# Performance work log

Measured on AMD Instinct MI355X. Metric: run time of the kernel, lower is better.

The kernel has to match this reference:

```python
import jax, jax.numpy as jnp
import numpy as np

HEAD_NUM = 16
NEG_BIG = -2.0**32 + 1.0


def _pos_encoding(T, D):
    pos = np.arange(T)[:, None].astype(np.float64)
    i = np.arange(D)[None, :].astype(np.float64)
    angle = pos / np.power(10000.0, 2.0 * i / D)
    pe = np.empty((T, D), dtype=np.float64)
    pe[:, 0::2] = np.sin(angle[:, 0::2])
    pe[:, 1::2] = np.cos(angle[:, 1::2])
    return jnp.asarray(pe * (D ** 0.5), dtype=jnp.float32)  # scale=True


def setup_inputs() -> dict:
    key = jax.random.key(0)
    ks = jax.random.split(key, 9)
    B, T, D = 32, 512, 1024
    return {
        "queries": jax.random.normal(ks[0], (B, T, D), jnp.float32),
        "keys": jax.random.normal(ks[1], (B, T, D), jnp.float32),
        "query_masks": jax.random.randint(ks[2], (B, 1), 1, T + 1, jnp.int32),
        "key_masks": jax.random.randint(ks[3], (B, 1), 1, T + 1, jnp.int32),
        "W_Query": jax.random.normal(ks[4], (D, D), jnp.float32) * 0.02,
        "W_key": jax.random.normal(ks[5], (D, D), jnp.float32) * 0.02,
        "W_Value": jax.random.normal(ks[6], (D, D), jnp.float32) * 0.02,
        "fw1": jax.random.normal(ks[7], (D, 4 * D), jnp.float32) * 0.02,
        "fw2": jax.random.normal(ks[8], (4 * D, D), jnp.float32) * 0.02,
    }


def reference(queries, keys, query_masks, key_masks, W_Query, W_key, W_Value, fw1, fw2):
    B, T, D = queries.shape
    h = HEAD_NUM
    d = D // h
    pe = _pos_encoding(T, D)  # [T, D]

    # faithful to source: queries get PE; keys = PE(queries_with_PE) (keys input unused)
    q_pe = queries + pe[None]
    k_pe = q_pe + pe[None]

    qs = jnp.einsum('btd,de->bte', q_pe, W_Query)
    ks_ = jnp.einsum('btd,de->bte', k_pe, W_key)
    vs = jnp.einsum('btd,de->bte', ks_, W_Value)  # faithful: values from projected keys

    def split_heads(x):  # [B,T,h*d] -> [h,B,T,d] (matches tf.split/concat on axis 0)
        return x.reshape(B, T, h, d).transpose(2, 0, 1, 3)

    q4, k4, v4 = split_heads(qs), split_heads(ks_), split_heads(vs)

    scores = jnp.einsum('hbqd,hbkd->hbqk', q4, k4) / (d ** 0.5)

    pos = jnp.arange(T)
    km = (pos[None, :] < key_masks).astype(jnp.float32)    # [B,T]
    qm = (pos[None, :] < query_masks).astype(jnp.float32)  # [B,T]

    scores = jnp.where(km[None, :, None, :] == 1.0, scores, NEG_BIG)
    scores = scores - jnp.max(scores, axis=-1, keepdims=True)
    attn = jax.nn.softmax(scores, axis=-1)
    attn = attn * qm[None, :, :, None]

    out = jnp.einsum('hbqk,hbkd->hbqd', attn, v4)
    result = out.transpose(1, 2, 0, 3).reshape(B, T, D)  # merge heads (head-major)

    result = result + q_pe  # use_res
    # feed forward (use_layer_norm=False, no dropout at inference)
    hmid = jax.nn.relu(jnp.einsum('btd,df->btf', result, fw1))
    result = result + jnp.einsum('btf,fd->btd', hmid, fw2)

    # output_type == 'mean'
    return jnp.mean(result, axis=1, keepdims=True)  # [B,1,D]
```

## Files before the change

kernel.cpp:

```cpp
#include <hip/hip_runtime.h>

constexpr int B_  = 32;
constexpr int T_  = 512;
constexpr int D_  = 1024;
constexpr int NH_ = 16;
constexpr int DH_ = 64;
constexpr int F_  = 4096;
constexpr int BT_ = B_ * T_;

typedef __attribute__((ext_vector_type(8))) short bf16x8;
typedef __attribute__((ext_vector_type(4))) float f32x4;

#define DEVI __device__ __forceinline__

DEVI unsigned short f2bf(float f) {
  union { float f; unsigned u; } uf; uf.f = f;
  unsigned r = uf.u + 0x7fffu + ((uf.u >> 16) & 1u);
  return (unsigned short)(r >> 16);
}
DEVI float b2f(unsigned short h) {
  union { unsigned u; float f; } uf; uf.u = ((unsigned)h) << 16;
  return uf.f;
}
DEVI void gload16(const void* g, void* l) {
  __builtin_amdgcn_global_load_lds(
      (const __attribute__((address_space(1))) void*)(uintptr_t)g,
      (__attribute__((address_space(3))) void*)(unsigned)(uintptr_t)l, 16, 0, 0);
}

__global__ void pe_kernel(float* __restrict__ pe) {
  int idx = blockIdx.x * 256 + threadIdx.x;
  int t = idx >> 10, j = idx & 1023;
  float inv = exp2f(-(2.0f * (float)j / 1024.0f) * 13.2877123795494f);
  float ang = (float)t * inv;
  float v = (j & 1) ? cosf(ang) : sinf(ang);
  pe[idx] = v * 32.0f;
}

__global__ void pack_kernel(const float* __restrict__ q, const float* __restrict__ pe,
                            unsigned short* __restrict__ q_pe, unsigned short* __restrict__ k_pe) {
  long i = ((long)blockIdx.x * 256 + threadIdx.x) * 4;
  const float4 qv = *(const float4*)(q + i);
  const float4 pv = *(const float4*)(pe + (i & (long)(T_ * D_ - 1)));
  ushort4 a, b;
  a.x = f2bf(qv.x + pv.x); a.y = f2bf(qv.y + pv.y);
  a.z = f2bf(qv.z + pv.z); a.w = f2bf(qv.w + pv.w);
  b.x = f2bf(qv.x + 2.f * pv.x); b.y = f2bf(qv.y + 2.f * pv.y);
  b.z = f2bf(qv.z + 2.f * pv.z); b.w = f2bf(qv.w + 2.f * pv.w);
  *(ushort4*)(q_pe + i) = a;
  *(ushort4*)(k_pe + i) = b;
}

__global__ void transpose_w(const float* __restrict__ W, unsigned short* __restrict__ Wt,
                            int K, int N) {
  __shared__ float tile[32][33];
  int tx = threadIdx.x & 31, ty = threadIdx.x >> 5;
  int bx = blockIdx.x, by = blockIdx.y;
  for (int i = 0; i < 4; i++) {
    int r = by * 32 + ty + i * 8;
    tile[ty + i * 8][tx] = W[(long)r * N + bx * 32 + tx];
  }
  __syncthreads();
  for (int i = 0; i < 4; i++) {
    int r = bx * 32 + ty + i * 8;
    Wt[(long)r * K + by * 32 + tx] = f2bf(tile[tx][ty + i * 8]);
  }
}

__global__ void cast_bf16(const float* __restrict__ W, unsigned short* __restrict__ Wb) {
  long i = ((long)blockIdx.x * 256 + threadIdx.x) * 4;
  const float4 v = *(const float4*)(W + i);
  ushort4 o;
  o.x = f2bf(v.x); o.y = f2bf(v.y); o.z = f2bf(v.z); o.w = f2bf(v.w);
  *(ushort4*)(Wb + i) = o;
}

template <int EPI>
__global__ __launch_bounds__(256) void gemm_bt(
    const unsigned short* __restrict__ A0, const unsigned short* __restrict__ Bt0,
    unsigned short* __restrict__ C0, float* __restrict__ hacc, int M, int N, int K) {
  __shared__ unsigned short As[128 * 32];
  __shared__ unsigned short Bs[128 * 32];
  const unsigned short* A  = A0;
  const unsigned short* Bt = Bt0;
  unsigned short* C        = C0;

  const int tid = threadIdx.x;
  const int lane = tid & 63, w = tid >> 6;
  const int wr = w >> 1, wc = w & 1;
  const int l15 = lane & 15, lhi = lane >> 4;
  const int brow = blockIdx.y * 128, bcol = blockIdx.x * 128;

  f32x4 acc[4][4] = {};
  const int o = tid * 16;
  const int srow = o >> 6;
  const int skel = (o & 63) >> 1;

  for (int kk = 0; kk < K; kk += 32) {
    gload16(A + (long)(brow + srow) * K + kk + skel,        (char*)As + o);
    gload16(A + (long)(brow + srow + 64) * K + kk + skel,   (char*)As + o + 4096);
    gload16(Bt + (long)(bcol + srow) * K + kk + skel,       (char*)Bs + o);
    gload16(Bt + (long)(bcol + srow + 64) * K + kk + skel,  (char*)Bs + o + 4096);
    __syncthreads();
    bf16x8 af[4], bfr[4];
    for (int m = 0; m < 4; m++)
      af[m] = *(const bf16x8*)((const char*)As + ((wr * 64 + m * 16 + l15) * 64 + lhi * 16));
    for (int n = 0; n < 4; n++)
      bfr[n] = *(const bf16x8*)((const char*)Bs + ((wc * 64 + n * 16 + l15) * 64 + lhi * 16));
    for (int m = 0; m < 4; m++)
      for (int n = 0; n < 4; n++)
        acc[m][n] = __builtin_amdgcn_mfma_f32_16x16x32_bf16(af[m], bfr[n], acc[m][n], 0, 0, 0);
    __syncthreads();
  }

  for (int m = 0; m < 4; m++)
    for (int n = 0; n < 4; n++) {
      int row = brow + wr * 64 + m * 16 + lhi * 4;
      int col = bcol + wc * 64 + n * 16 + l15;
      for (int r = 0; r < 4; r++)
        C[(long)(row + r) * N + col] = f2bf(acc[m][n][r]);
    }
}

template <int EPI>
__global__ __launch_bounds__(512, 2) void gemm8(
    const unsigned short* __restrict__ A0, const unsigned short* __restrict__ Bt0, unsigned short* __restrict__ C0,
    const unsigned short* __restrict__ A1, const unsigned short* __restrict__ Bt1, unsigned short* __restrict__ C1,
    const unsigned short* __restrict__ A2, const unsigned short* __restrict__ Bt2, unsigned short* __restrict__ C2,
    float* __restrict__ hacc, int N,
    const int* __restrict__ L0, const int* __restrict__ L1, const int* __restrict__ L2) {
  constexpr int K = 1024, NK = 16, NI = 8;
  __shared__ char lds[2][2][32768];

  const int z = blockIdx.z;
  const unsigned short* A  = (z == 0) ? A0  : (z == 1 ? A1  : A2);
  const unsigned short* Bt = (z == 0) ? Bt0 : (z == 1 ? Bt1 : Bt2);
  unsigned short* C        = (z == 0) ? C0  : (z == 1 ? C1  : C2);
  const int* L             = (z == 0) ? L0  : (z == 1 ? L1  : L2);

  const long brow = (long)blockIdx.x * 256, bcol = (long)blockIdx.y * 256;
  if (L && (brow & 256) && L[brow >> 9] <= 256) return;

  const int tid = threadIdx.x;
  const int lane = tid & 63, w = tid >> 6;
  const int wm = w >> 2, wn = w & 3;
  const int l15 = lane & 15, lhi = lane >> 4;

  const int drow = (tid * 16) >> 7;
  const int dcol = ((tid * 16) & 127) ^ ((drow & 7) << 4);
  const int sw   = (l15 & 7) << 4;

  f32x4 acc[8][4] = {};
  bf16x8 bfr[4][2], af[2][2];

  auto STAGE = [&](const unsigned short* __restrict__ P, long tb, int kt, int h, int buf, int op) {
    const unsigned short* g = P + (tb + h * 128 + drow) * (long)K + kt * 64 + (dcol >> 1);
    char* l = &lds[buf][op][h * 16384 + tid * 16];
    gload16(g, l);
    gload16(g + 64L * K, l + 8192);
  };
  auto LDA = [&](int buf, int q) {
#pragma unroll
    for (int mi = 0; mi < 2; mi++) {
      int row = wm * 128 + (q * 2 + mi) * 16 + l15;
#pragma unroll
      for (int kk = 0; kk < 2; kk++)
        af[mi][kk] = *(const bf16x8*)(&lds[buf][0][0] + (row << 7) + ((kk * 64 + lhi * 16) ^ sw));
    }
  };
  auto LDB = [&](int buf) {
#pragma unroll
    for (int n = 0; n < 4; n++) {
      int row = wn * 64 + n * 16 + l15;
#pragma unroll
      for (int kk = 0; kk < 2; kk++)
        bfr[n][kk] = *(const bf16x8*)(&lds[buf][1][0] + (row << 7) + ((kk * 64 + lhi * 16) ^ sw));
    }
  };
  auto MFMAQ = [&](int q) {
    __builtin_amdgcn_s_setprio(1);
#pragma unroll
    for (int mi = 0; mi < 2; mi++)
#pragma unroll
      for (int n = 0; n < 4; n++)
#pragma unroll
        for (int kk = 0; kk < 2; kk++)
          acc[q * 2 + mi][n] =
              __builtin_amdgcn_mfma_f32_16x16x32_bf16(af[mi][kk], bfr[n][kk], acc[q * 2 + mi][n], 0, 0, 0);
    __builtin_amdgcn_s_setprio(0);
  };
#define BAR() __builtin_amdgcn_s_barrier()
#define GATE4() asm volatile("s_waitcnt vmcnt(4)" ::: "memory")

  STAGE(A, brow, 0, 0, 0, 0);  STAGE(A, brow, 0, 1, 0, 0);
  STAGE(Bt, bcol, 0, 0, 0, 1); STAGE(Bt, bcol, 0, 1, 0, 1);
  STAGE(Bt, bcol, 1, 0, 1, 1); STAGE(Bt, bcol, 1, 1, 1, 1);
  GATE4();
  BAR();

  for (int i = 0; i < NI; ++i) {
    const int k1 = 2 * i + 1;
    const int ka = (2 * i + 2) & (NK - 1);
    const int kb = (2 * i + 3) & (NK - 1);
    LDA(0, 0); LDB(0); STAGE(A, brow, k1, 0, 1, 0);
    BAR(); MFMAQ(0); BAR();
    LDA(0, 1);         STAGE(A, brow, k1, 1, 1, 0);
    BAR(); MFMAQ(1); BAR();
    LDA(0, 2);         STAGE(Bt, bcol, ka, 0, 0, 1);
    BAR(); MFMAQ(2); BAR();
    LDA(0, 3);         STAGE(Bt, bcol, ka, 1, 0, 1);
    BAR(); MFMAQ(3);
    GATE4();
    BAR();
    LDA(1, 0); LDB(1); STAGE(A, brow, ka, 0, 0, 0);
    BAR(); MFMAQ(0); BAR();
    LDA(1, 1);         STAGE(A, brow, ka, 1, 0, 0);
    BAR(); MFMAQ(1); BAR();
    LDA(1, 2);         STAGE(Bt, bcol, kb, 0, 1, 1);
    BAR(); MFMAQ(2); BAR();
    LDA(1, 3);         STAGE(Bt, bcol, kb, 1, 1, 1);
    BAR(); MFMAQ(3);
    GATE4();
    BAR();
  }
#undef BAR
#undef GATE4

  if (EPI == 0) {
    if (z == 2) {
      char* tl = &lds[0][0][0] + (w << 14);
#pragma unroll
      for (int m = 0; m < 8; m++)
#pragma unroll
        for (int n = 0; n < 4; n++) {
          int cl = n * 16 + l15;
#pragma unroll
          for (int r = 0; r < 4; r++) {
            int tofs = m * 16 + lhi * 4 + r;
            *(unsigned short*)(tl + cl * 256 + ((tofs * 2) ^ ((cl & 7) << 4))) = f2bf(acc[m][n][r]);
          }
        }
      asm volatile("" ::: "memory");
      const int bb = (int)(brow >> 9), t0 = (int)(brow & 511);
#pragma unroll
      for (int rr = 0; rr < 16; rr++) {
        int row = rr * 4 + lhi;
        bf16x8 v = *(const bf16x8*)(tl + row * 256 + ((l15 * 16) ^ ((row & 7) << 4)));
        int gcol = (int)bcol + wn * 64 + row;
        long vtrow = ((long)(bb * NH_ + (gcol >> 6))) * DH_ + (gcol & 63);
        *(bf16x8*)(C + vtrow * T_ + t0 + wm * 128 + l15 * 8) = v;
      }
    } else {
#pragma unroll
      for (int m = 0; m < 8; m++)
#pragma unroll
        for (int n = 0; n < 4; n++) {
          long row = brow + wm * 128 + m * 16 + lhi * 4;
          long col = bcol + wn * 64 + n * 16 + l15;
#pragma unroll
          for (int r = 0; r < 4; r++)
            C[(row + r) * (long)N + col] = f2bf(acc[m][n][r]);
        }
    }
  } else {
    const int batch = (int)(brow >> 9);
#pragma unroll
    for (int n = 0; n < 4; n++) {
      float t = 0.f;
#pragma unroll
      for (int m = 0; m < 8; m++)
#pragma unroll
        for (int r = 0; r < 4; r++) t += fmaxf(acc[m][n][r], 0.f);
      t += __shfl_xor(t, 16);
      t += __shfl_xor(t, 32);
      if (lane < 16)
        atomicAdd(hacc + (long)batch * F_ + bcol + wn * 64 + n * 16 + l15, t);
    }
  }
}

__global__ __launch_bounds__(256, 3) void attn_kernel(
    const unsigned short* __restrict__ qs, const unsigned short* __restrict__ ks,
    const unsigned short* __restrict__ vt, const unsigned short* __restrict__ q_pe,
    const int* __restrict__ qmask, const int* __restrict__ kmask,
    unsigned short* __restrict__ res, float* __restrict__ racc) {
  __shared__ unsigned short Ks[2][64 * 64];
  __shared__ unsigned short Vs[2][64 * 64];
  __shared__ unsigned short Ps[4][32 * 64];

  const int tid = threadIdx.x, lane = tid & 63, w = tid >> 6;
  const int l15 = lane & 15, lhi = lane >> 4;
  const int h = blockIdx.x, b = blockIdx.y, q0 = blockIdx.z * 128;
  const int qlen = qmask[b], kvlen = kmask[b];

  if (q0 >= qlen) {
    int cc = tid & 63;
    float s = 0.f;
    for (int i = 0; i < 32; i++) {
      int r = (tid >> 6) * 32 + i;
      long addr = (long)(b * T_ + q0 + r) * D_ + h * DH_ + cc;
      unsigned short v = q_pe[addr];
      res[addr] = v;
      s += b2f(v);
    }
    atomicAdd(racc + b * D_ + h * DH_ + cc, s);
    return;
  }

  bf16x8 qf[2][2];
  for (int m = 0; m < 2; m++)
    for (int k2 = 0; k2 < 2; k2++) {
      int t = q0 + w * 32 + m * 16 + l15;
      qf[m][k2] = *(const bf16x8*)(qs + (long)(b * T_ + t) * D_ + h * DH_ + k2 * 32 + lhi * 8);
    }

  f32x4 o[2][4] = {};
  float mrun[2][4], lrun[2][4];
  for (int m = 0; m < 2; m++)
    for (int r = 0; r < 4; r++) { mrun[m][r] = -3e38f; lrun[m][r] = 0.f; }

  const float SCL = 0.125f * 1.4426950408889634f;
  const float THR = 8.0f / SCL;
  const int nc = (kvlen + 63) >> 6;

  auto stage = [&](int c, int buf) {
#pragma unroll
    for (int cl = 0; cl < 2; cl++) {
      int ob = cl * 4096 + tid * 16;
      int os = ob ^ (((ob >> 7) & 7) << 4);
      int r0 = os >> 7, cb = os & 127;
      gload16(ks + (long)(b * T_ + c * 64 + r0) * D_ + h * DH_ + (cb >> 1),
              (char*)&Ks[buf][0] + ob);
      gload16(vt + ((long)(b * NH_ + h) * DH_ + r0) * T_ + c * 64 + (cb >> 1),
              (char*)&Vs[buf][0] + ob);
    }
  };

  stage(0, 0);
  int cur = 0;
  for (int c = 0; c < nc; c++) {
    const int nxt = (c + 1 < nc) ? c + 1 : c;
    stage(nxt, cur ^ 1);
    asm volatile("s_waitcnt vmcnt(4)" ::: "memory");
    __builtin_amdgcn_sched_barrier(0);
    __builtin_amdgcn_s_barrier();

    f32x4 s[2][4] = {};
    for (int k2 = 0; k2 < 2; k2++)
      for (int n = 0; n < 4; n++) {
        int key = n * 16 + l15;
        int Ab = key * 128 + (k2 * 32 + lhi * 8) * 2;
        bf16x8 kf = *(const bf16x8*)((const char*)&Ks[cur][0] + (Ab ^ ((key & 7) << 4)));
        s[0][n] = __builtin_amdgcn_mfma_f32_16x16x32_bf16(qf[0][k2], kf, s[0][n], 0, 0, 0);
        s[1][n] = __builtin_amdgcn_mfma_f32_16x16x32_bf16(qf[1][k2], kf, s[1][n], 0, 0, 0);
      }

    if (c == nc - 1) {
      for (int n = 0; n < 4; n++)
        if (c * 64 + n * 16 + l15 >= kvlen)
          for (int m = 0; m < 2; m++) s[m][n] = f32x4{-3e38f, -3e38f, -3e38f, -3e38f};
    }

    for (int m = 0; m < 2; m++) {
      float mx[4];
      for (int r = 0; r < 4; r++) {
        float v = s[m][0][r];
        for (int n = 1; n < 4; n++) v = fmaxf(v, s[m][n][r]);
        mx[r] = v;
      }
      for (int msk = 1; msk < 16; msk <<= 1)
        for (int r = 0; r < 4; r++) mx[r] = fmaxf(mx[r], __shfl_xor(mx[r], msk));
      bool grow = false;
      for (int r = 0; r < 4; r++) grow = grow || (mx[r] > mrun[m][r] + THR);
      if (__any(grow)) {
        float corr[4];
        for (int r = 0; r < 4; r++) {
          float mn = fmaxf(mrun[m][r], mx[r]);
          corr[r] = exp2f((mrun[m][r] - mn) * SCL);
          mrun[m][r] = mn;
        }
        for (int nd = 0; nd < 4; nd++)
          for (int r = 0; r < 4; r++) o[m][nd][r] *= corr[r];
        for (int r = 0; r < 4; r++) lrun[m][r] *= corr[r];
      }
      float ps[4] = {0.f, 0.f, 0.f, 0.f};
      for (int n = 0; n < 4; n++)
        for (int r = 0; r < 4; r++) {
          float pval = exp2f((s[m][n][r] - mrun[m][r]) * SCL);
          s[m][n][r] = pval;
          ps[r] += pval;
        }
      for (int msk = 1; msk < 16; msk <<= 1)
        for (int r = 0; r < 4; r++) ps[r] += __shfl_xor(ps[r], msk);
      for (int r = 0; r < 4; r++) lrun[m][r] += ps[r];
      for (int n = 0; n < 4; n++)
        for (int r = 0; r < 4; r++) {
          int row = m * 16 + lhi * 4 + r;
          int Ab = row * 128 + (n * 16 + l15) * 2;
          *(unsigned short*)((char*)&Ps[w][0] + (Ab ^ ((row & 7) << 4))) = f2bf(s[m][n][r]);
        }
    }
    asm volatile("" ::: "memory");

    for (int k4 = 0; k4 < 2; k4++) {
      bf16x8 pa[2];
      for (int m = 0; m < 2; m++) {
        int row = m * 16 + l15;
        int Ab = row * 128 + k4 * 64 + lhi * 16;
        pa[m] = *(const bf16x8*)((const char*)&Ps[w][0] + (Ab ^ ((row & 7) << 4)));
      }
      for (int nd = 0; nd < 4; nd++) {
        int dv = nd * 16 + l15;
        int Ab = dv * 128 + k4 * 64 + lhi * 16;
        bf16x8 vb = *(const bf16x8*)((const char*)&Vs[cur][0] + (Ab ^ ((dv & 7) << 4)));
        for (int m = 0; m < 2; m++)
          o[m][nd] = __builtin_amdgcn_mfma_f32_16x16x32_bf16(pa[m], vb, o[m][nd], 0, 0, 0);
      }
    }
    __builtin_amdgcn_s_barrier();
    cur ^= 1;
  }

  float cs[4] = {0.f, 0.f, 0.f, 0.f};
  for (int m = 0; m < 2; m++)
    for (int r = 0; r < 4; r++) {
      int t = q0 + w * 32 + m * 16 + lhi * 4 + r;
      float inv = 1.0f / lrun[m][r];
      bool valid = t < qlen;
      for (int nd = 0; nd < 4; nd++) {
        long addr = (long)(b * T_ + t) * D_ + h * DH_ + nd * 16 + l15;
        float v = valid ? o[m][nd][r] * inv : 0.f;
        float val = v + b2f(q_pe[addr]);
        res[addr] = f2bf(val);
        cs[nd] += val;
      }
    }
  for (int nd = 0; nd < 4; nd++) {
    cs[nd] += __shfl_xor(cs[nd], 16);
    cs[nd] += __shfl_xor(cs[nd], 32);
  }
  if (lane < 16)
    for (int nd = 0; nd < 4; nd++)
      atomicAdd(racc + b * D_ + h * DH_ + nd * 16 + l15, cs[nd]);
}

__global__ void final_kernel(const float* __restrict__ hacc, const float* __restrict__ fw2,
                             const float* __restrict__ racc, float* __restrict__ out) {
  int n = blockIdx.x * 64 + (threadIdx.x & 63);
  int bg = threadIdx.x >> 6;
  int f0 = blockIdx.y * 512;
  float acc[8] = {};
  for (int f = f0; f < f0 + 512; f++) {
    float wv = fw2[(long)f * D_ + n];
    for (int i = 0; i < 8; i++) acc[i] += hacc[(long)(bg * 8 + i) * F_ + f] * wv;
  }
  if (blockIdx.y == 0)
    for (int i = 0; i < 8; i++) acc[i] += racc[(long)(bg * 8 + i) * D_ + n];
  for (int i = 0; i < 8; i++)
    atomicAdd(out + (bg * 8 + i) * D_ + n, acc[i] * (1.0f / 512.0f));
}

extern "C" void kernel_launch(void* const* d_in, const int* in_sizes, int n_in,
                              void* d_out, int out_size, void* d_ws, size_t ws_size,
                              hipStream_t stream) {
  const float* queries = (const float*)d_in[0];
  const int*   qmask = (const int*)d_in[2];
  const int*   kmask = (const int*)d_in[3];
  const float* Wq  = (const float*)d_in[4];
  const float* Wk  = (const float*)d_in[5];
  const float* Wv  = (const float*)d_in[6];
  const float* fw1 = (const float*)d_in[7];
  const float* fw2 = (const float*)d_in[8];
  float* out = (float*)d_out;

  char* p = (char*)d_ws;
  auto alloc = [&](size_t bytes) -> char* {
    char* r = p; p += (bytes + 255) & ~(size_t)255; return r;
  };
  float*          pe   = (float*)alloc((size_t)T_ * D_ * 4);
  unsigned short* q_pe = (unsigned short*)alloc((size_t)BT_ * D_ * 2);
  unsigned short* k_pe = (unsigned short*)alloc((size_t)BT_ * D_ * 2);
  unsigned short* qs   = (unsigned short*)alloc((size_t)BT_ * D_ * 2);
  unsigned short* ksb  = (unsigned short*)alloc((size_t)BT_ * D_ * 2);
  unsigned short* vt   = (unsigned short*)alloc((size_t)BT_ * D_ * 2);
  unsigned short* res  = (unsigned short*)alloc((size_t)BT_ * D_ * 2);
  unsigned short* Wqt  = (unsigned short*)alloc((size_t)D_ * D_ * 2);
  unsigned short* Wkt  = (unsigned short*)alloc((size_t)D_ * D_ * 2);
  unsigned short* Wvt  = (unsigned short*)alloc((size_t)D_ * D_ * 2);
  unsigned short* Wkbf = (unsigned short*)alloc((size_t)D_ * D_ * 2);
  unsigned short* Wkvt = (unsigned short*)alloc((size_t)D_ * D_ * 2);
  unsigned short* fw1t = (unsigned short*)alloc((size_t)D_ * F_ * 2);
  float*          racc = (float*)alloc((size_t)B_ * D_ * 4);
  float*          hacc = (float*)alloc((size_t)B_ * F_ * 4);

  hipMemsetAsync(hacc, 0, (size_t)B_ * F_ * 4, stream);
  hipMemsetAsync(racc, 0, (size_t)B_ * D_ * 4, stream);
  hipMemsetAsync(out, 0, (size_t)B_ * D_ * 4, stream);

  pe_kernel<<<T_ * D_ / 256, 256, 0, stream>>>(pe);
  pack_kernel<<<BT_ * D_ / 1024, 256, 0, stream>>>(queries, pe, q_pe, k_pe);
  transpose_w<<<dim3(32, 32), 256, 0, stream>>>(Wq, Wqt, D_, D_);
  transpose_w<<<dim3(32, 32), 256, 0, stream>>>(Wk, Wkt, D_, D_);
  transpose_w<<<dim3(32, 32), 256, 0, stream>>>(Wv, Wvt, D_, D_);
  transpose_w<<<dim3(F_ / 32, 32), 256, 0, stream>>>(fw1, fw1t, D_, F_);
  cast_bf16<<<(D_ * D_) / 1024, 256, 0, stream>>>(Wk, Wkbf);

  gemm_bt<0><<<dim3(8, 8, 1), 256, 0, stream>>>(Wvt, Wkbf, Wkvt, nullptr, D_, D_, D_);

  gemm8<0><<<dim3(64, 4, 3), 512, 0, stream>>>(q_pe, Wqt, qs,
                                               k_pe, Wkt, ksb,
                                               k_pe, Wkvt, vt,
                                               nullptr, D_, qmask, kmask, kmask);

  attn_kernel<<<dim3(16, 32, 4), 256, 0, stream>>>(qs, ksb, vt, q_pe, qmask, kmask, res, racc);

  gemm8<1><<<dim3(64, 16, 1), 512, 0, stream>>>(res, fw1t, nullptr,
                                                res, fw1t, nullptr,
                                                res, fw1t, nullptr,
                                                hacc, F_, nullptr, nullptr, nullptr);

  final_kernel<<<dim3(16, 8), 256, 0, stream>>>(hacc, fw2, racc, out);
}
```

Before: 416.1 us.

## Merge weight prep launches, swap FFN GEMM grid order, add epilogue barrier

Five weight transpose/cast launches are merged into one prep kernel with a z-indexed grid, and the Wk bf16 cast is folded into the Wk transpose. The FFN GEMM grid swaps its block axes so consecutive blocks walk across columns of the same row panel, which may improve L2 reuse of activations. A vmcnt wait plus a barrier is added before the z==2 epilogue reuses LDS, guarding against in-flight loads corrupting the transpose buffer. The merged prep launch has many idle early-exit blocks.

```diff
diff --git a/kernel.cpp b/kernel.cpp
--- a/kernel.cpp
+++ b/kernel.cpp
@@ -51,28 +51,30 @@
   *(ushort4*)(k_pe + i) = b;
 }
 
-__global__ void transpose_w(const float* __restrict__ W, unsigned short* __restrict__ Wt,
-                            int K, int N) {
+__global__ void prep_w(const float* __restrict__ Wq, const float* __restrict__ Wk,
+                       const float* __restrict__ Wv, const float* __restrict__ fw1,
+                       unsigned short* __restrict__ Wqt, unsigned short* __restrict__ Wkt,
+                       unsigned short* __restrict__ Wvt, unsigned short* __restrict__ fw1t,
+                       unsigned short* __restrict__ Wkbf) {
+  const int z = blockIdx.z;
+  if (z < 3 && blockIdx.x >= 32) return;
+  const float* W = (z == 0) ? Wq : (z == 1) ? Wk : (z == 2) ? Wv : fw1;
+  unsigned short* Wt = (z == 0) ? Wqt : (z == 1) ? Wkt : (z == 2) ? Wvt : fw1t;
+  const int N = (z == 3) ? F_ : D_;
   __shared__ float tile[32][33];
   int tx = threadIdx.x & 31, ty = threadIdx.x >> 5;
   int bx = blockIdx.x, by = blockIdx.y;
   for (int i = 0; i < 4; i++) {
     int r = by * 32 + ty + i * 8;
-    tile[ty + i * 8][tx] = W[(long)r * N + bx * 32 + tx];
+    float v = W[(long)r * N + bx * 32 + tx];
+    tile[ty + i * 8][tx] = v;
+    if (z == 1) Wkbf[(long)r * D_ + bx * 32 + tx] = f2bf(v);
   }
   __syncthreads();
   for (int i = 0; i < 4; i++) {
     int r = bx * 32 + ty + i * 8;
-    Wt[(long)r * K + by * 32 + tx] = f2bf(tile[tx][ty + i * 8]);
-  }
-}
-
-__global__ void cast_bf16(const float* __restrict__ W, unsigned short* __restrict__ Wb) {
-  long i = ((long)blockIdx.x * 256 + threadIdx.x) * 4;
-  const float4 v = *(const float4*)(W + i);
-  ushort4 o;
-  o.x = f2bf(v.x); o.y = f2bf(v.y); o.z = f2bf(v.z); o.w = f2bf(v.w);
-  *(ushort4*)(Wb + i) = o;
+    Wt[(long)r * D_ + by * 32 + tx] = f2bf(tile[tx][ty + i * 8]);
+  }
 }
 
 template <int EPI>
@@ -122,7 +124,7 @@
     }
 }
 
-template <int EPI>
+template <int EPI, int GSWAP>
 __global__ __launch_bounds__(512, 2) void gemm8(
     const unsigned short* __restrict__ A0, const unsigned short* __restrict__ Bt0, unsigned short* __restrict__ C0,
     const unsigned short* __restrict__ A1, const unsigned short* __restrict__ Bt1, unsigned short* __restrict__ C1,
@@ -138,7 +140,8 @@
   unsigned short* C        = (z == 0) ? C0  : (z == 1 ? C1  : C2);
   const int* L             = (z == 0) ? L0  : (z == 1 ? L1  : L2);
 
-  const long brow = (long)blockIdx.x * 256, bcol = (long)blockIdx.y * 256;
+  const long brow = (long)(GSWAP ? blockIdx.y : blockIdx.x) * 256;
+  const long bcol = (long)(GSWAP ? blockIdx.x : blockIdx.y) * 256;
   if (L && (brow & 256) && L[brow >> 9] <= 256) return;
 
   const int tid = threadIdx.x;
@@ -228,6 +231,8 @@
 
   if (EPI == 0) {
     if (z == 2) {
+      asm volatile("s_waitcnt vmcnt(0)" ::: "memory");
+      __builtin_amdgcn_s_barrier();
       char* tl = &lds[0][0][0] + (w << 14);
 #pragma unroll
       for (int m = 0; m < 8; m++)
@@ -499,25 +504,21 @@
 
   pe_kernel<<<T_ * D_ / 256, 256, 0, stream>>>(pe);
   pack_kernel<<<BT_ * D_ / 1024, 256, 0, stream>>>(queries, pe, q_pe, k_pe);
-  transpose_w<<<dim3(32, 32), 256, 0, stream>>>(Wq, Wqt, D_, D_);
-  transpose_w<<<dim3(32, 32), 256, 0, stream>>>(Wk, Wkt, D_, D_);
-  transpose_w<<<dim3(32, 32), 256, 0, stream>>>(Wv, Wvt, D_, D_);
-  transpose_w<<<dim3(F_ / 32, 32), 256, 0, stream>>>(fw1, fw1t, D_, F_);
-  cast_bf16<<<(D_ * D_) / 1024, 256, 0, stream>>>(Wk, Wkbf);
+  prep_w<<<dim3(128, 32, 4), 256, 0, stream>>>(Wq, Wk, Wv, fw1, Wqt, Wkt, Wvt, fw1t, Wkbf);
 
   gemm_bt<0><<<dim3(8, 8, 1), 256, 0, stream>>>(Wvt, Wkbf, Wkvt, nullptr, D_, D_, D_);
 
-  gemm8<0><<<dim3(64, 4, 3), 512, 0, stream>>>(q_pe, Wqt, qs,
-                                               k_pe, Wkt, ksb,
-                                               k_pe, Wkvt, vt,
-                                               nullptr, D_, qmask, kmask, kmask);
+  gemm8<0, 0><<<dim3(64, 4, 3), 512, 0, stream>>>(q_pe, Wqt, qs,
+                                                  k_pe, Wkt, ksb,
+                                                  k_pe, Wkvt, vt,
+                                                  nullptr, D_, qmask, kmask, kmask);
 
   attn_kernel<<<dim3(16, 32, 4), 256, 0, stream>>>(qs, ksb, vt, q_pe, qmask, kmask, res, racc);
 
-  gemm8<1><<<dim3(64, 16, 1), 512, 0, stream>>>(res, fw1t, nullptr,
-                                                res, fw1t, nullptr,
-                                                res, fw1t, nullptr,
-                                                hacc, F_, nullptr, nullptr, nullptr);
+  gemm8<1, 1><<<dim3(16, 64, 1), 512, 0, stream>>>(res, fw1t, nullptr,
+                                                   res, fw1t, nullptr,
+                                                   res, fw1t, nullptr,
+                                                   hacc, F_, nullptr, nullptr, nullptr);
 
   final_kernel<<<dim3(16, 8), 256, 0, stream>>>(hacc, fw2, racc, out);
 }
```

Measured after the change: 415.8 us. Within noise of the previous version (-0.1%).
